# Kernel tuning notes

Hardware: AMD Instinct MI355X
Metric: run time of the kernel (lower is better)

Reference implementation:

```python
import math
import jax, jax.numpy as jnp
import numpy as np

B, H, Nt, Nl, E = 4, 16, 512, 512, 64
P = H * E  # 1024, pre-projection embedding dim


def setup_inputs() -> dict:
    key = jax.random.key(0)
    ks = jax.random.split(key, 8)
    return {
        "projected_u": jax.random.normal(ks[0], (B, H, Nt, P), jnp.float32),
        "projected_b": jax.random.normal(ks[1], (B, H, Nt, 1), jnp.float32),
        "mu": jax.random.normal(ks[2], (B, Nl, P), jnp.float32),
        "logvar": jax.random.normal(ks[3], (B, Nl, P), jnp.float32) * 0.5,
        "pi": jax.random.uniform(ks[4], (B, Nl, 1), jnp.float32, 1e-3, 1.0),
        "w_v": jax.random.normal(ks[5], (H, E, P), jnp.float32) * 0.02,
        "b_v": jax.random.normal(ks[6], (H, E, Nl), jnp.float32) * 0.02,
        "attn_mask": jnp.zeros((B * H, 1, Nl), dtype=bool),  # True = masked
    }


def reference(projected_u, projected_b, mu, logvar, pi, w_v, b_v, attn_mask):
    Bq, Hq, Ntq, Pq = projected_u.shape
    Nlq = mu.shape[1]
    Eq = w_v.shape[1]
    prior_var_u = math.sqrt(Eq)

    var = jnp.exp(logvar)                         # [B,Nl,P]
    biased_var = var + prior_var_u                # [B,Nl,P]

    # float additive mask [B*H,1,Nl]: -inf where attn_mask True or pi<=0
    pi_rep = jnp.repeat(pi, Hq, axis=0)           # [B*H,Nl,1]
    am = jnp.where(attn_mask, -jnp.inf, 0.0)
    am = am + jnp.where(pi_rep.transpose(0, 2, 1) <= 0, -jnp.inf, 0.0)
    masked = jnp.isneginf(am).transpose(0, 2, 1)  # [B*H,Nl,1]

    # scores [B,H,Nt,Nl]
    attn = jnp.einsum('bhmp,bnp->bhmn', projected_u, mu / biased_var) + projected_b

    pi_c = jnp.maximum(pi_rep, jnp.finfo(pi_rep.dtype).tiny)
    t1 = jnp.where(masked, 0.0, jnp.log(pi_c))                                  # [B*H,Nl,1]
    t2 = 0.5 * jnp.sum((mu / jnp.sqrt(biased_var)) ** 2, axis=-1, keepdims=True)  # [B,Nl,1]
    t2 = jnp.repeat(t2, Hq, axis=0)                                             # [B*H,Nl,1]
    t3 = jnp.where(masked, 0.0, jnp.log(jnp.repeat(biased_var, Hq, axis=0)))    # [B*H,Nl,P]
    t3 = jnp.sum(0.5 * t3, axis=-1, keepdims=True)                              # [B*H,Nl,1]

    attn = attn + (t1 - t2 - t3).reshape(Bq, Hq, Nlq, 1).transpose(0, 1, 3, 2)  # [B,H,1,Nl]
    attn = attn + am.reshape(Bq, Hq, 1, Nlq)
    attn = jax.nn.softmax(attn, axis=-1)                                        # [B,H,Nt,Nl]

    # denoised values: interpolation between query projection and means
    out = (jnp.einsum('bhmn,bnp->bhmp', attn, var / biased_var) * projected_u
           + jnp.einsum('bhmn,bnp->bhmp', attn, (prior_var_u / biased_var) * mu))  # [B,H,Nt,P]
    out = (jnp.einsum('bhmp,hep->bhme', out, w_v)
           + jnp.einsum('bhmn,hen->bhme', attn, b_v))                              # [B,H,Nt,E]
    return (out.reshape(Bq * Hq, Ntq, Eq), attn.reshape(Bq * Hq, Ntq, Nlq))
```

## Files before the change

kernel.cpp:

```cpp
#include <hip/hip_runtime.h>
#include <cstdint>
#include <cstddef>
#include <cmath>

#define B_  4
#define H_  16
#define NT  512
#define NL  512
#define E_  64
#define P_  1024
#define HE  1024
#define BH  64

typedef __attribute__((ext_vector_type(8))) short short8;
typedef __attribute__((ext_vector_type(4))) float f32x4;
typedef unsigned short u16;

#define MFMA(a, b, c) __builtin_amdgcn_mfma_f32_16x16x32_bf16(a, b, c, 0, 0, 0)

static __device__ inline u16 f2bf_rne(float f) {
  unsigned u = __float_as_uint(f);
  unsigned r = u + 0x7FFFu + ((u >> 16) & 1u);
  return (u16)(r >> 16);
}

static __device__ inline void gl_lds16(const void* g, void* l) {
  __builtin_amdgcn_global_load_lds(
      (const __attribute__((address_space(1))) void*)g,
      (__attribute__((address_space(3))) void*)l, 16, 0, 0);
}

__global__ __launch_bounds__(256) void k_precompute(
    const float* __restrict__ mu, const float* __restrict__ logvar,
    const float* __restrict__ pi, u16* __restrict__ mobv_hi,
    u16* __restrict__ mobv_lo, u16* __restrict__ ibvT,
    float* __restrict__ bias) {
  const int bn = blockIdx.x;
  const int b = bn >> 9, n = bn & 511;
  const int t = threadIdx.x;
  const size_t base = (size_t)bn * P_;
  float t2 = 0.f, t3 = 0.f;
#pragma unroll
  for (int i = 0; i < P_ / 256; ++i) {
    const int p = t + i * 256;
    const float lv  = logvar[base + p];
    const float v   = expf(lv);
    const float bv  = v + 8.0f;
    const float inv = 1.0f / bv;
    const float m   = mu[base + p];
    const float x   = m * inv;
    const unsigned bits = __float_as_uint(x);
    mobv_hi[base + p] = (u16)(bits >> 16);
    const float r = x - __uint_as_float(bits & 0xFFFF0000u);
    mobv_lo[base + p] = (u16)(__float_as_uint(r) >> 16);
    ibvT[((size_t)b * P_ + p) * NL + n] = f2bf_rne(inv);
    t2 += m * x;
    t3 += logf(bv);
  }
  __shared__ float r2[256];
  __shared__ float r3[256];
  r2[t] = t2; r3[t] = t3;
  __syncthreads();
  for (int s = 128; s > 0; s >>= 1) {
    if (t < s) { r2[t] += r2[t + s]; r3[t] += r3[t + s]; }
    __syncthreads();
  }
  if (t == 0) {
    const float pv = pi[bn];
    float bb;
    if (pv <= 0.f) bb = -INFINITY;
    else bb = logf(fmaxf(pv, 1.17549435e-38f)) - 0.5f * r2[0] - 0.5f * r3[0];
    bias[bn] = bb;
  }
}

__global__ __launch_bounds__(256) void k_wvcast(const float* __restrict__ wv,
                                                u16* __restrict__ wvb) {
  const int i = (blockIdx.x * 256 + threadIdx.x) * 4;
  const float4 f = *(const float4*)&wv[i];
  wvb[i + 0] = f2bf_rne(f.x);
  wvb[i + 1] = f2bf_rne(f.y);
  wvb[i + 2] = f2bf_rne(f.z);
  wvb[i + 3] = f2bf_rne(f.w);
}

__global__ __launch_bounds__(256) void k_w2p(
    const u16* __restrict__ mobv_hi, const u16* __restrict__ mobv_lo,
    const u16* __restrict__ wvb, const float* __restrict__ bv_,
    u16* __restrict__ W2pT) {
  const int b    = blockIdx.z;
  const int row0 = blockIdx.x * 64;
  const int col0 = blockIdx.y * 128;
  const int t = threadIdx.x;
  const int wave = t >> 6, lane = t & 63;
  const int l16 = lane & 15, sel = lane >> 4;
  const int mrow = (wave >> 1) * 32, ncol = (wave & 1) * 64;

  __shared__ u16 Ah[64 * 32];
  __shared__ u16 Al[64 * 32];
  __shared__ u16 Bs[128 * 32];

  const u16* Abh = mobv_hi + ((size_t)b * NL + row0) * P_;
  const u16* Abl = mobv_lo + ((size_t)b * NL + row0) * P_;
  const u16* Bb  = wvb + (size_t)col0 * P_;

  f32x4 acc[2][4];
#pragma unroll
  for (int i = 0; i < 2; ++i)
#pragma unroll
    for (int j = 0; j < 4; ++j) acc[i][j] = (f32x4){0.f, 0.f, 0.f, 0.f};

  for (int k0 = 0; k0 < P_; k0 += 32) {
    {
      const int c = t;
      const int row = c >> 2, k8 = (c & 3) ^ ((row >> 1) & 3);
      gl_lds16(Abh + (size_t)row * P_ + k0 + k8 * 8, &Ah[wave * 64 * 8]);
      gl_lds16(Abl + (size_t)row * P_ + k0 + k8 * 8, &Al[wave * 64 * 8]);
    }
#pragma unroll
    for (int i = 0; i < 2; ++i) {
      const int c = t + i * 256;
      const int row = c >> 2, k8 = (c & 3) ^ ((row >> 1) & 3);
      gl_lds16(Bb + (size_t)row * P_ + k0 + k8 * 8,
               &Bs[(i * 256 + wave * 64) * 8]);
    }
    __syncthreads();
    short8 ah[2], al[2], bf[4];
#pragma unroll
    for (int mt = 0; mt < 2; ++mt) {
      const int r = mrow + mt * 16 + l16;
      const int ch = sel ^ ((r >> 1) & 3);
      ah[mt] = *(const short8*)&Ah[r * 32 + ch * 8];
      al[mt] = *(const short8*)&Al[r * 32 + ch * 8];
    }
#pragma unroll
    for (int nt = 0; nt < 4; ++nt) {
      const int r = ncol + nt * 16 + l16;
      const int ch = sel ^ ((r >> 1) & 3);
      bf[nt] = *(const short8*)&Bs[r * 32 + ch * 8];
    }
#pragma unroll
    for (int mt = 0; mt < 2; ++mt)
#pragma unroll
      for (int nt = 0; nt < 4; ++nt) {
        acc[mt][nt] = MFMA(ah[mt], bf[nt], acc[mt][nt]);
        acc[mt][nt] = MFMA(al[mt], bf[nt], acc[mt][nt]);
      }
    __syncthreads();
  }
#pragma unroll
  for (int mt = 0; mt < 2; ++mt) {
    const int nbase = row0 + mrow + mt * 16 + sel * 4;
#pragma unroll
    for (int nt = 0; nt < 4; ++nt) {
      const int he = col0 + ncol + nt * 16 + l16;
      const float4 bvv = *(const float4*)&bv_[(size_t)he * NL + nbase];
      ushort4 o;
      o.x = f2bf_rne(8.0f * acc[mt][nt][0] + bvv.x);
      o.y = f2bf_rne(8.0f * acc[mt][nt][1] + bvv.y);
      o.z = f2bf_rne(8.0f * acc[mt][nt][2] + bvv.z);
      o.w = f2bf_rne(8.0f * acc[mt][nt][3] + bvv.w);
      *(ushort4*)&W2pT[((size_t)b * HE + he) * NL + nbase] = o;
    }
  }
}

__global__ __launch_bounds__(256) void k_scores(
    const float* __restrict__ U, const u16* __restrict__ mobv_hi,
    const u16* __restrict__ mobv_lo, const float* __restrict__ pb,
    const float* __restrict__ bias, const uint8_t* __restrict__ mask,
    float* __restrict__ attn) {
  const int b    = blockIdx.z;
  const int row0 = blockIdx.x * 128;
  const int col0 = blockIdx.y * 128;
  const int t = threadIdx.x;
  const int wave = t >> 6, lane = t & 63;
  const int l16 = lane & 15, sel = lane >> 4;
  const int mrow = (wave >> 1) * 64, ncol = (wave & 1) * 64;

  __shared__ float Af[128 * 32];
  __shared__ u16   Bh[128 * 32];
  __shared__ u16   Bl[128 * 32];

  const float* Ab  = U + ((size_t)b * 8192 + row0) * P_;
  const u16*   Bbh = mobv_hi + ((size_t)b * NL + col0) * P_;
  const u16*   Bbl = mobv_lo + ((size_t)b * NL + col0) * P_;

  f32x4 acc[4][4];
#pragma unroll
  for (int i = 0; i < 4; ++i)
#pragma unroll
    for (int j = 0; j < 4; ++j) acc[i][j] = (f32x4){0.f, 0.f, 0.f, 0.f};

  for (int k0 = 0; k0 < P_; k0 += 32) {
#pragma unroll
    for (int i = 0; i < 4; ++i) {
      const int c = t + i * 256;
      const int row = c >> 3, k4 = (c & 7) ^ (row & 7);
      gl_lds16(Ab + (size_t)row * P_ + k0 + k4 * 4,
               &Af[(i * 256 + wave * 64) * 4]);
    }
#pragma unroll
    for (int i = 0; i < 2; ++i) {
      const int c = t + i * 256;
      const int row = c >> 2, k8 = (c & 3) ^ ((row >> 1) & 3);
      gl_lds16(Bbh + (size_t)row * P_ + k0 + k8 * 8,
               &Bh[(i * 256 + wave * 64) * 8]);
      gl_lds16(Bbl + (size_t)row * P_ + k0 + k8 * 8,
               &Bl[(i * 256 + wave * 64) * 8]);
    }
    __syncthreads();

    short8 ah[4], al[4], bh[4], bl[4];
#pragma unroll
    for (int mt = 0; mt < 4; ++mt) {
      const int r = mrow + mt * 16 + l16;
      const int c0 = (sel * 2) ^ (r & 7);
      const int c1 = (sel * 2 + 1) ^ (r & 7);
      const float4 f0 = *(const float4*)&Af[r * 32 + c0 * 4];
      const float4 f1 = *(const float4*)&Af[r * 32 + c1 * 4];
      const float fv[8] = {f0.x, f0.y, f0.z, f0.w, f1.x, f1.y, f1.z, f1.w};
#pragma unroll
      for (int j = 0; j < 8; ++j) {
        const unsigned bits = __float_as_uint(fv[j]);
        ah[mt][j] = (short)(bits >> 16);
        const float rr = fv[j] - __uint_as_float(bits & 0xFFFF0000u);
        al[mt][j] = (short)(__float_as_uint(rr) >> 16);
      }
    }
#pragma unroll
    for (int nt = 0; nt < 4; ++nt) {
      const int r = ncol + nt * 16 + l16;
      const int ch = sel ^ ((r >> 1) & 3);
      bh[nt] = *(const short8*)&Bh[r * 32 + ch * 8];
      bl[nt] = *(const short8*)&Bl[r * 32 + ch * 8];
    }
#pragma unroll
    for (int mt = 0; mt < 4; ++mt)
#pragma unroll
      for (int nt = 0; nt < 4; ++nt) {
        acc[mt][nt] = MFMA(ah[mt], bh[nt], acc[mt][nt]);
        acc[mt][nt] = MFMA(ah[mt], bl[nt], acc[mt][nt]);
        acc[mt][nt] = MFMA(al[mt], bh[nt], acc[mt][nt]);
      }
    __syncthreads();
  }

  const int bh_ = b * H_ + (row0 >> 9);
  float pbv[4][4];
#pragma unroll
  for (int mt = 0; mt < 4; ++mt)
#pragma unroll
    for (int r = 0; r < 4; ++r)
      pbv[mt][r] = pb[(size_t)b * 8192 + row0 + mrow + mt * 16 + sel * 4 + r];
#pragma unroll
  for (int nt = 0; nt < 4; ++nt) {
    const int n = col0 + ncol + nt * 16 + l16;
    const float bcol = bias[b * NL + n];
    const bool mk = mask[(size_t)bh_ * NL + n] != 0;
#pragma unroll
    for (int mt = 0; mt < 4; ++mt) {
#pragma unroll
      for (int r = 0; r < 4; ++r) {
        const int row = row0 + mrow + mt * 16 + sel * 4 + r;
        float s = acc[mt][nt][r] + pbv[mt][r] + bcol;
        if (mk) s = -INFINITY;
        attn[((size_t)b * 8192 + row) * NL + n] = s;
      }
    }
  }
}

__global__ __launch_bounds__(256) void k_softmax(float* __restrict__ attn,
                                                 u16* __restrict__ attn_bf) {
  const size_t r = blockIdx.x;
  float* row = attn + r * NL;
  const int t = threadIdx.x;
  float2 v = ((float2*)row)[t];
  __shared__ float red[256];
  red[t] = fmaxf(v.x, v.y);
  __syncthreads();
  for (int s = 128; s > 0; s >>= 1) {
    if (t < s) red[t] = fmaxf(red[t], red[t + s]);
    __syncthreads();
  }
  const float M = red[0];
  __syncthreads();
  const float e0 = expf(v.x - M);
  const float e1 = expf(v.y - M);
  red[t] = e0 + e1;
  __syncthreads();
  for (int s = 128; s > 0; s >>= 1) {
    if (t < s) red[t] += red[t + s];
    __syncthreads();
  }
  const float inv = 1.0f / red[0];
  float2 o; o.x = e0 * inv; o.y = e1 * inv;
  ((float2*)row)[t] = o;
  ushort2 ob; ob.x = f2bf_rne(o.x); ob.y = f2bf_rne(o.y);
  ((ushort2*)(attn_bf + r * NL))[t] = ob;
}

__global__ __launch_bounds__(256) void k_mid(
    const u16* __restrict__ attn_bf, const u16* __restrict__ ibvT,
    const float* __restrict__ U, u16* __restrict__ opS) {
  const int b    = blockIdx.z;
  const int row0 = blockIdx.x * 128;
  const int col0 = blockIdx.y * 128;
  const int t = threadIdx.x;
  const int wave = t >> 6, lane = t & 63;
  const int l16 = lane & 15, sel = lane >> 4;
  const int mrow = (wave >> 1) * 64, ncol = (wave & 1) * 64;

  __shared__ u16 As[128 * 32];
  __shared__ u16 Bs[128 * 32];

  const u16* Ab = attn_bf + ((size_t)b * 8192 + row0) * NL;
  const u16* Bb = ibvT + ((size_t)b * P_ + col0) * NL;

  f32x4 acc[4][4];
#pragma unroll
  for (int i = 0; i < 4; ++i)
#pragma unroll
    for (int j = 0; j < 4; ++j) acc[i][j] = (f32x4){0.f, 0.f, 0.f, 0.f};

  for (int k0 = 0; k0 < NL; k0 += 32) {
#pragma unroll
    for (int i = 0; i < 2; ++i) {
      const int c = t + i * 256;
      const int row = c >> 2, k8 = (c & 3) ^ ((row >> 1) & 3);
      gl_lds16(Ab + (size_t)row * NL + k0 + k8 * 8,
               &As[(i * 256 + wave * 64) * 8]);
      gl_lds16(Bb + (size_t)row * NL + k0 + k8 * 8,
               &Bs[(i * 256 + wave * 64) * 8]);
    }
    __syncthreads();
    short8 af[4], bf[4];
#pragma unroll
    for (int mt = 0; mt < 4; ++mt) {
      const int r = mrow + mt * 16 + l16;
      const int ch = sel ^ ((r >> 1) & 3);
      af[mt] = *(const short8*)&As[r * 32 + ch * 8];
    }
#pragma unroll
    for (int nt = 0; nt < 4; ++nt) {
      const int r = ncol + nt * 16 + l16;
      const int ch = sel ^ ((r >> 1) & 3);
      bf[nt] = *(const short8*)&Bs[r * 32 + ch * 8];
    }
#pragma unroll
    for (int mt = 0; mt < 4; ++mt)
#pragma unroll
      for (int nt = 0; nt < 4; ++nt)
        acc[mt][nt] = MFMA(af[mt], bf[nt], acc[mt][nt]);
    __syncthreads();
  }

#pragma unroll
  for (int mt = 0; mt < 4; ++mt) {
#pragma unroll
    for (int r = 0; r < 4; ++r) {
      const int m = row0 + mrow + mt * 16 + sel * 4 + r;
      const float* Urow = U + ((size_t)b * 8192 + m) * P_;
      u16* orow = opS + ((size_t)b * 8192 + m) * P_;
#pragma unroll
      for (int nt = 0; nt < 4; ++nt) {
        const int p = col0 + ncol + nt * 16 + l16;
        const float u = Urow[p];
        orow[p] = f2bf_rne((1.0f - 8.0f * acc[mt][nt][r]) * u);
      }
    }
  }
}

__global__ __launch_bounds__(256) void k_out2(
    const u16* __restrict__ opS, const u16* __restrict__ attn_bf,
    const u16* __restrict__ wvb, const u16* __restrict__ W2pT,
    float* __restrict__ out) {
  const int bh = blockIdx.y;
  const int b = bh >> 4, h = bh & 15;
  const int row0g = bh * NT + blockIdx.x * 64;
  const int t = threadIdx.x;
  const int wave = t >> 6, lane = t & 63;
  const int l16 = lane & 15, sel = lane >> 4;
  const int mrow = (wave >> 1) * 32, ncol = (wave & 1) * 32;

  __shared__ u16 As[64 * 32];
  __shared__ u16 Bs[64 * 32];

  f32x4 acc[2][2];
#pragma unroll
  for (int i = 0; i < 2; ++i)
#pragma unroll
    for (int j = 0; j < 2; ++j) acc[i][j] = (f32x4){0.f, 0.f, 0.f, 0.f};

  const u16* Ab1 = opS + (size_t)row0g * P_;
  const u16* Bb1 = wvb + (size_t)(h * 64) * P_;
  for (int k0 = 0; k0 < P_; k0 += 32) {
    const int c = t;
    const int row = c >> 2, k8 = (c & 3) ^ ((row >> 1) & 3);
    gl_lds16(Ab1 + (size_t)row * P_ + k0 + k8 * 8, &As[(wave * 64) * 8]);
    gl_lds16(Bb1 + (size_t)row * P_ + k0 + k8 * 8, &Bs[(wave * 64) * 8]);
    __syncthreads();
    short8 af[2], bf[2];
#pragma unroll
    for (int mt = 0; mt < 2; ++mt) {
      const int r = mrow + mt * 16 + l16;
      const int ch = sel ^ ((r >> 1) & 3);
      af[mt] = *(const short8*)&As[r * 32 + ch * 8];
    }
#pragma unroll
    for (int nt = 0; nt < 2; ++nt) {
      const int r = ncol + nt * 16 + l16;
      const int ch = sel ^ ((r >> 1) & 3);
      bf[nt] = *(const short8*)&Bs[r * 32 + ch * 8];
    }
#pragma unroll
    for (int mt = 0; mt < 2; ++mt)
#pragma unroll
      for (int nt = 0; nt < 2; ++nt)
        acc[mt][nt] = MFMA(af[mt], bf[nt], acc[mt][nt]);
    __syncthreads();
  }

  const u16* Ab2 = attn_bf + (size_t)row0g * NL;
  const u16* Bb2 = W2pT + ((size_t)b * HE + h * 64) * NL;
  for (int k0 = 0; k0 < NL; k0 += 32) {
    const int c = t;
    const int row = c >> 2, k8 = (c & 3) ^ ((row >> 1) & 3);
    gl_lds16(Ab2 + (size_t)row * NL + k0 + k8 * 8, &As[(wave * 64) * 8]);
    gl_lds16(Bb2 + (size_t)row * NL + k0 + k8 * 8, &Bs[(wave * 64) * 8]);
    __syncthreads();
    short8 af[2], bf[2];
#pragma unroll
    for (int mt = 0; mt < 2; ++mt) {
      const int r = mrow + mt * 16 + l16;
      const int ch = sel ^ ((r >> 1) & 3);
      af[mt] = *(const short8*)&As[r * 32 + ch * 8];
    }
#pragma unroll
    for (int nt = 0; nt < 2; ++nt) {
      const int r = ncol + nt * 16 + l16;
      const int ch = sel ^ ((r >> 1) & 3);
      bf[nt] = *(const short8*)&Bs[r * 32 + ch * 8];
    }
#pragma unroll
    for (int mt = 0; mt < 2; ++mt)
#pragma unroll
      for (int nt = 0; nt < 2; ++nt)
        acc[mt][nt] = MFMA(af[mt], bf[nt], acc[mt][nt]);
    __syncthreads();
  }

#pragma unroll
  for (int mt = 0; mt < 2; ++mt)
#pragma unroll
    for (int nt = 0; nt < 2; ++nt)
#pragma unroll
      for (int r = 0; r < 4; ++r) {
        const int row = row0g + mrow + mt * 16 + sel * 4 + r;
        const int e = ncol + nt * 16 + l16;
        out[(size_t)row * E_ + e] = acc[mt][nt][r];
      }
}

extern "C" void kernel_launch(void* const* d_in, const int* in_sizes, int n_in,
                              void* d_out, int out_size, void* d_ws, size_t ws_size,
                              hipStream_t stream) {
  const float*   u    = (const float*)d_in[0];
  const float*   pb   = (const float*)d_in[1];
  const float*   mu   = (const float*)d_in[2];
  const float*   logv = (const float*)d_in[3];
  const float*   pi   = (const float*)d_in[4];
  const float*   wv   = (const float*)d_in[5];
  const float*   bv   = (const float*)d_in[6];
  const uint8_t* mask = (const uint8_t*)d_in[7];

  float* out  = (float*)d_out;
  float* attn = out + (size_t)BH * NT * E_;

  u16*   mobv_hi = (u16*)d_ws;
  u16*   mobv_lo = mobv_hi + (size_t)B_ * NL * P_;
  u16*   ibvT    = mobv_lo + (size_t)B_ * NL * P_;
  u16*   W2pT    = ibvT + (size_t)B_ * P_ * NL;
  u16*   wvb     = W2pT + (size_t)B_ * HE * NL;
  float* bias    = (float*)(wvb + (size_t)HE * P_);
  u16*   attn_bf = (u16*)(bias + (size_t)B_ * NL);
  u16*   opS     = attn_bf + (size_t)BH * NT * NL;

  k_precompute<<<B_ * NL, 256, 0, stream>>>(mu, logv, pi, mobv_hi, mobv_lo,
                                            ibvT, bias);
  k_wvcast<<<(HE * P_) / 1024, 256, 0, stream>>>(wv, wvb);
  k_w2p<<<dim3(NL / 64, HE / 128, B_), 256, 0, stream>>>(mobv_hi, mobv_lo, wvb,
                                                         bv, W2pT);
  k_scores<<<dim3(8192 / 128, NL / 128, B_), 256, 0, stream>>>(
      u, mobv_hi, mobv_lo, pb, bias, mask, attn);
  k_softmax<<<B_ * H_ * NT, 256, 0, stream>>>(attn, attn_bf);
  k_mid<<<dim3(8192 / 128, P_ / 128, B_), 256, 0, stream>>>(attn_bf, ibvT, u,
                                                            opS);
  k_out2<<<dim3(NT / 64, BH), 256, 0, stream>>>(opS, attn_bf, wvb, W2pT, out);
}
```

Before: 485.8 us.

## Split fp32 A into bf16 hi/lo once in scores, wave-per-row softmax, K=64 out2 tiles

In k_scores, each thread now loads fp32 U directly into registers, splits it into bf16 hi/lo parts once, and stores both to LDS. Previously every wave re-split the fp32 tile after reading it from LDS, so the split is no longer repeated across the two column waves. The softmax now uses one wavefront per row with shuffle reductions instead of a block-wide shared-memory tree with many barriers. k_out2 doubles its K tile to 64, halving loop iterations and barriers. The trade-offs are that the A loads become synchronous register loads instead of async global-to-LDS copies, and LDS use grows.

```diff
diff --git a/kernel.cpp b/kernel.cpp
--- a/kernel.cpp
+++ b/kernel.cpp
@@ -178,13 +178,24 @@
   const int l16 = lane & 15, sel = lane >> 4;
   const int mrow = (wave >> 1) * 64, ncol = (wave & 1) * 64;
 
-  __shared__ float Af[128 * 32];
-  __shared__ u16   Bh[128 * 32];
-  __shared__ u16   Bl[128 * 32];
-
-  const float* Ab  = U + ((size_t)b * 8192 + row0) * P_;
-  const u16*   Bbh = mobv_hi + ((size_t)b * NL + col0) * P_;
-  const u16*   Bbl = mobv_lo + ((size_t)b * NL + col0) * P_;
+  __shared__ u16 Ah[128 * 32];
+  __shared__ u16 Al[128 * 32];
+  __shared__ u16 Bh[128 * 32];
+  __shared__ u16 Bl[128 * 32];
+
+  const u16* Bbh = mobv_hi + ((size_t)b * NL + col0) * P_;
+  const u16* Bbl = mobv_lo + ((size_t)b * NL + col0) * P_;
+
+  const int arow = t >> 1;
+  const int ak   = (t & 1) * 16;
+  const float* Aptr = U + ((size_t)b * 8192 + row0 + arow) * P_ + ak;
+  const int asw = (arow >> 1) & 3;
+  const int ch0 = ((t & 1) * 2 + 0) ^ asw;
+  const int ch1 = ((t & 1) * 2 + 1) ^ asw;
+  u16* AhW0 = &Ah[arow * 32 + ch0 * 8];
+  u16* AhW1 = &Ah[arow * 32 + ch1 * 8];
+  u16* AlW0 = &Al[arow * 32 + ch0 * 8];
+  u16* AlW1 = &Al[arow * 32 + ch1 * 8];
 
   f32x4 acc[4][4];
 #pragma unroll
@@ -193,13 +204,10 @@
     for (int j = 0; j < 4; ++j) acc[i][j] = (f32x4){0.f, 0.f, 0.f, 0.f};
 
   for (int k0 = 0; k0 < P_; k0 += 32) {
-#pragma unroll
-    for (int i = 0; i < 4; ++i) {
-      const int c = t + i * 256;
-      const int row = c >> 3, k4 = (c & 7) ^ (row & 7);
-      gl_lds16(Ab + (size_t)row * P_ + k0 + k4 * 4,
-               &Af[(i * 256 + wave * 64) * 4]);
-    }
+    const float4 a0 = *(const float4*)&Aptr[k0 + 0];
+    const float4 a1 = *(const float4*)&Aptr[k0 + 4];
+    const float4 a2 = *(const float4*)&Aptr[k0 + 8];
+    const float4 a3 = *(const float4*)&Aptr[k0 + 12];
 #pragma unroll
     for (int i = 0; i < 2; ++i) {
       const int c = t + i * 256;
@@ -209,24 +217,33 @@
       gl_lds16(Bbl + (size_t)row * P_ + k0 + k8 * 8,
                &Bl[(i * 256 + wave * 64) * 8]);
     }
+    const float av[16] = {a0.x, a0.y, a0.z, a0.w, a1.x, a1.y, a1.z, a1.w,
+                          a2.x, a2.y, a2.z, a2.w, a3.x, a3.y, a3.z, a3.w};
+    short8 h0, h1, l0, l1;
+#pragma unroll
+    for (int j = 0; j < 8; ++j) {
+      unsigned bits = __float_as_uint(av[j]);
+      h0[j] = (short)(bits >> 16);
+      float rr = av[j] - __uint_as_float(bits & 0xFFFF0000u);
+      l0[j] = (short)(__float_as_uint(rr) >> 16);
+      bits = __float_as_uint(av[8 + j]);
+      h1[j] = (short)(bits >> 16);
+      rr = av[8 + j] - __uint_as_float(bits & 0xFFFF0000u);
+      l1[j] = (short)(__float_as_uint(rr) >> 16);
+    }
+    *(short8*)AhW0 = h0;
+    *(short8*)AhW1 = h1;
+    *(short8*)AlW0 = l0;
+    *(short8*)AlW1 = l1;
     __syncthreads();
 
     short8 ah[4], al[4], bh[4], bl[4];
 #pragma unroll
     for (int mt = 0; mt < 4; ++mt) {
       const int r = mrow + mt * 16 + l16;
-      const int c0 = (sel * 2) ^ (r & 7);
-      const int c1 = (sel * 2 + 1) ^ (r & 7);
-      const float4 f0 = *(const float4*)&Af[r * 32 + c0 * 4];
-      const float4 f1 = *(const float4*)&Af[r * 32 + c1 * 4];
-      const float fv[8] = {f0.x, f0.y, f0.z, f0.w, f1.x, f1.y, f1.z, f1.w};
-#pragma unroll
-      for (int j = 0; j < 8; ++j) {
-        const unsigned bits = __float_as_uint(fv[j]);
-        ah[mt][j] = (short)(bits >> 16);
-        const float rr = fv[j] - __uint_as_float(bits & 0xFFFF0000u);
-        al[mt][j] = (short)(__float_as_uint(rr) >> 16);
-      }
+      const int ch = sel ^ ((r >> 1) & 3);
+      ah[mt] = *(const short8*)&Ah[r * 32 + ch * 8];
+      al[mt] = *(const short8*)&Al[r * 32 + ch * 8];
     }
 #pragma unroll
     for (int nt = 0; nt < 4; ++nt) {
@@ -273,32 +290,37 @@
 
 __global__ __launch_bounds__(256) void k_softmax(float* __restrict__ attn,
                                                  u16* __restrict__ attn_bf) {
-  const size_t r = blockIdx.x;
+  const int t = threadIdx.x;
+  const int wave = t >> 6, lane = t & 63;
+  const size_t r = (size_t)blockIdx.x * 4 + wave;
   float* row = attn + r * NL;
-  const int t = threadIdx.x;
-  float2 v = ((float2*)row)[t];
-  __shared__ float red[256];
-  red[t] = fmaxf(v.x, v.y);
-  __syncthreads();
-  for (int s = 128; s > 0; s >>= 1) {
-    if (t < s) red[t] = fmaxf(red[t], red[t + s]);
-    __syncthreads();
-  }
-  const float M = red[0];
-  __syncthreads();
-  const float e0 = expf(v.x - M);
-  const float e1 = expf(v.y - M);
-  red[t] = e0 + e1;
-  __syncthreads();
-  for (int s = 128; s > 0; s >>= 1) {
-    if (t < s) red[t] += red[t + s];
-    __syncthreads();
-  }
-  const float inv = 1.0f / red[0];
-  float2 o; o.x = e0 * inv; o.y = e1 * inv;
-  ((float2*)row)[t] = o;
-  ushort2 ob; ob.x = f2bf_rne(o.x); ob.y = f2bf_rne(o.y);
-  ((ushort2*)(attn_bf + r * NL))[t] = ob;
+  const float4 v0 = ((const float4*)row)[lane * 2];
+  const float4 v1 = ((const float4*)row)[lane * 2 + 1];
+  float m = fmaxf(fmaxf(fmaxf(v0.x, v0.y), fmaxf(v0.z, v0.w)),
+                  fmaxf(fmaxf(v1.x, v1.y), fmaxf(v1.z, v1.w)));
+#pragma unroll
+  for (int off = 32; off > 0; off >>= 1) m = fmaxf(m, __shfl_xor(m, off, 64));
+  float e[8];
+  e[0] = expf(v0.x - m); e[1] = expf(v0.y - m);
+  e[2] = expf(v0.z - m); e[3] = expf(v0.w - m);
+  e[4] = expf(v1.x - m); e[5] = expf(v1.y - m);
+  e[6] = expf(v1.z - m); e[7] = expf(v1.w - m);
+  float s = ((e[0] + e[1]) + (e[2] + e[3])) + ((e[4] + e[5]) + (e[6] + e[7]));
+#pragma unroll
+  for (int off = 32; off > 0; off >>= 1) s += __shfl_xor(s, off, 64);
+  const float inv = 1.0f / s;
+  float4 o0, o1;
+  o0.x = e[0] * inv; o0.y = e[1] * inv; o0.z = e[2] * inv; o0.w = e[3] * inv;
+  o1.x = e[4] * inv; o1.y = e[5] * inv; o1.z = e[6] * inv; o1.w = e[7] * inv;
+  ((float4*)row)[lane * 2] = o0;
+  ((float4*)row)[lane * 2 + 1] = o1;
+  ushort4 b0, b1;
+  b0.x = f2bf_rne(o0.x); b0.y = f2bf_rne(o0.y);
+  b0.z = f2bf_rne(o0.z); b0.w = f2bf_rne(o0.w);
+  b1.x = f2bf_rne(o1.x); b1.y = f2bf_rne(o1.y);
+  b1.z = f2bf_rne(o1.z); b1.w = f2bf_rne(o1.w);
+  ((ushort4*)(attn_bf + r * NL))[lane * 2] = b0;
+  ((ushort4*)(attn_bf + r * NL))[lane * 2 + 1] = b1;
 }
 
 __global__ __launch_bounds__(256) void k_mid(
@@ -385,8 +407,8 @@
   const int l16 = lane & 15, sel = lane >> 4;
   const int mrow = (wave >> 1) * 32, ncol = (wave & 1) * 32;
 
-  __shared__ u16 As[64 * 32];
-  __shared__ u16 Bs[64 * 32];
+  __shared__ u16 As[64 * 64];
+  __shared__ u16 Bs[64 * 64];
 
   f32x4 acc[2][2];
 #pragma unroll
@@ -396,59 +418,85 @@
 
   const u16* Ab1 = opS + (size_t)row0g * P_;
   const u16* Bb1 = wvb + (size_t)(h * 64) * P_;
-  for (int k0 = 0; k0 < P_; k0 += 32) {
-    const int c = t;
-    const int row = c >> 2, k8 = (c & 3) ^ ((row >> 1) & 3);
-    gl_lds16(Ab1 + (size_t)row * P_ + k0 + k8 * 8, &As[(wave * 64) * 8]);
-    gl_lds16(Bb1 + (size_t)row * P_ + k0 + k8 * 8, &Bs[(wave * 64) * 8]);
-    __syncthreads();
-    short8 af[2], bf[2];
+  for (int k0 = 0; k0 < P_; k0 += 64) {
+#pragma unroll
+    for (int i = 0; i < 2; ++i) {
+      const int c = t + i * 256;
+      const int row = c >> 3, k8 = (c & 7) ^ (row & 7);
+      gl_lds16(Ab1 + (size_t)row * P_ + k0 + k8 * 8,
+               &As[(i * 256 + wave * 64) * 8]);
+      gl_lds16(Bb1 + (size_t)row * P_ + k0 + k8 * 8,
+               &Bs[(i * 256 + wave * 64) * 8]);
+    }
+    __syncthreads();
+    short8 af[2][2], bf[2][2];
 #pragma unroll
     for (int mt = 0; mt < 2; ++mt) {
       const int r = mrow + mt * 16 + l16;
-      const int ch = sel ^ ((r >> 1) & 3);
-      af[mt] = *(const short8*)&As[r * 32 + ch * 8];
+#pragma unroll
+      for (int kk = 0; kk < 2; ++kk) {
+        const int ch = (kk * 4 + sel) ^ (r & 7);
+        af[mt][kk] = *(const short8*)&As[r * 64 + ch * 8];
+      }
     }
 #pragma unroll
     for (int nt = 0; nt < 2; ++nt) {
       const int r = ncol + nt * 16 + l16;
-      const int ch = sel ^ ((r >> 1) & 3);
-      bf[nt] = *(const short8*)&Bs[r * 32 + ch * 8];
+#pragma unroll
+      for (int kk = 0; kk < 2; ++kk) {
+        const int ch = (kk * 4 + sel) ^ (r & 7);
+        bf[nt][kk] = *(const short8*)&Bs[r * 64 + ch * 8];
+      }
     }
 #pragma unroll
     for (int mt = 0; mt < 2; ++mt)
 #pragma unroll
-      for (int nt = 0; nt < 2; ++nt)
-        acc[mt][nt] = MFMA(af[mt], bf[nt], acc[mt][nt]);
+      for (int nt = 0; nt < 2; ++nt) {
+        acc[mt][nt] = MFMA(af[mt][0], bf[nt][0], acc[mt][nt]);
+        acc[mt][nt] = MFMA(af[mt][1], bf[nt][1], acc[mt][nt]);
+      }
     __syncthreads();
   }
 
   const u16* Ab2 = attn_bf + (size_t)row0g * NL;
   const u16* Bb2 = W2pT + ((size_t)b * HE + h * 64) * NL;
-  for (int k0 = 0; k0 < NL; k0 += 32) {
-    const int c = t;
-    const int row = c >> 2, k8 = (c & 3) ^ ((row >> 1) & 3);
-    gl_lds16(Ab2 + (size_t)row * NL + k0 + k8 * 8, &As[(wave * 64) * 8]);
-    gl_lds16(Bb2 + (size_t)row * NL + k0 + k8 * 8, &Bs[(wave * 64) * 8]);
-    __syncthreads();
-    short8 af[2], bf[2];
+  for (int k0 = 0; k0 < NL; k0 += 64) {
+#pragma unroll
+    for (int i = 0; i < 2; ++i) {
+      const int c = t + i * 256;
+      const int row = c >> 3, k8 = (c & 7) ^ (row & 7);
+      gl_lds16(Ab2 + (size_t)row * NL + k0 + k8 * 8,
+               &As[(i * 256 + wave * 64) * 8]);
+      gl_lds16(Bb2 + (size_t)row * NL + k0 + k8 * 8,
+               &Bs[(i * 256 + wave * 64) * 8]);
+    }
+    __syncthreads();
+    short8 af[2][2], bf[2][2];
 #pragma unroll
     for (int mt = 0; mt < 2; ++mt) {
       const int r = mrow + mt * 16 + l16;
-      const int ch = sel ^ ((r >> 1) & 3);
-      af[mt] = *(const short8*)&As[r * 32 + ch * 8];
+#pragma unroll
+      for (int kk = 0; kk < 2; ++kk) {
+        const int ch = (kk * 4 + sel) ^ (r & 7);
+        af[mt][kk] = *(const short8*)&As[r * 64 + ch * 8];
+      }
     }
 #pragma unroll
     for (int nt = 0; nt < 2; ++nt) {
       const int r = ncol + nt * 16 + l16;
-      const int ch = sel ^ ((r >> 1) & 3);
-      bf[nt] = *(const short8*)&Bs[r * 32 + ch * 8];
+#pragma unroll
+      for (int kk = 0; kk < 2; ++kk) {
+        const int ch = (kk * 4 + sel) ^ (r & 7);
+        bf[nt][kk] = *(const short8*)&Bs[r * 64 + ch * 8];
+      }
     }
 #pragma unroll
     for (int mt = 0; mt < 2; ++mt)
 #pragma unroll
-      for (int nt = 0; nt < 2; ++nt)
-        acc[mt][nt] = MFMA(af[mt], bf[nt], acc[mt][nt]);
+      for (int nt = 0; nt < 2; ++nt) {
+        acc[mt][nt] = MFMA(af[mt][0], bf[nt][0], acc[mt][nt]);
+        acc[mt][nt] = MFMA(af[mt][1], bf[nt][1], acc[mt][nt]);
+      }
     __syncthreads();
   }
 
@@ -495,7 +543,7 @@
                                                          bv, W2pT);
   k_scores<<<dim3(8192 / 128, NL / 128, B_), 256, 0, stream>>>(
       u, mobv_hi, mobv_lo, pb, bias, mask, attn);
-  k_softmax<<<B_ * H_ * NT, 256, 0, stream>>>(attn, attn_bf);
+  k_softmax<<<(B_ * H_ * NT) / 4, 256, 0, stream>>>(attn, attn_bf);
   k_mid<<<dim3(8192 / 128, P_ / 128, B_), 256, 0, stream>>>(attn_bf, ibvT, u,
                                                             opS);
   k_out2<<<dim3(NT / 64, BH), 256, 0, stream>>>(opS, attn_bf, wvb, W2pT, out);
```

After: 489.1 us. About the same (+0.7%).
